# Kernel tuning notes

Measured on AMD Instinct MI355X. Metric: run time of the kernel, lower is better.

Reference implementation:

```python
import jax, jax.numpy as jnp
import numpy as np

N_NODES = 10000
N_EDGES = 160000
F_IN, D1, D2, D_OUT, K = 512, 512, 512, 256, 3


def _gcn_layer(x, row, col, w, W, b, n):
    # PyG GCNConv (improved=False): add self-loops with weight 1, sym norm.
    loop = jnp.arange(n)
    r = jnp.concatenate([row, loop])
    c = jnp.concatenate([col, loop])
    ww = jnp.concatenate([w, jnp.ones((n,), w.dtype)])
    deg = jax.ops.segment_sum(ww, c, num_segments=n)
    dinv = jnp.where(deg > 0, jax.lax.rsqrt(deg), 0.0)
    norm = dinv[r] * ww * dinv[c]              # [E+N]
    h = x @ W                                  # dense GEMM first (as PyG lin)
    out = jax.ops.segment_sum(norm[:, None] * h[r], c, num_segments=n)
    return out + b


def _cheb_layer(x, row, col, w, Wk, b, n):
    # PyG ChebConv, normalization='sym', lambda_max=2.0:
    # L_hat = 2L/lmax - I = -D^{-1/2} A D^{-1/2} (self-loops removed first).
    w0 = jnp.where(row == col, jnp.zeros((), w.dtype), w)  # remove self loops
    deg = jax.ops.segment_sum(w0, row, num_segments=n)
    dinv = jnp.where(deg > 0, jax.lax.rsqrt(deg), 0.0)
    norm = dinv[row] * w0 * dinv[col]          # [E]

    def lhat(z):  # L_hat @ z
        return -jax.ops.segment_sum(norm[:, None] * z[row], col, num_segments=n)

    Tx0 = x
    out = Tx0 @ Wk[0]
    Tx1 = lhat(x)
    out = out + Tx1 @ Wk[1]
    for k in range(2, Wk.shape[0]):            # static K, fine to unroll
        Tx2 = 2.0 * lhat(Tx1) - Tx0
        out = out + Tx2 @ Wk[k]
        Tx0, Tx1 = Tx1, Tx2
    return out + b


def setup_inputs() -> dict:
    key = jax.random.key(0)
    ks = jax.random.split(key, 9)
    x = jax.random.normal(ks[0], (N_NODES, F_IN), dtype=jnp.float32)
    edge_index = jax.random.randint(ks[1], (2, N_EDGES), 0, N_NODES, dtype=jnp.int64)
    edge_weight = jax.random.uniform(ks[2], (N_EDGES,), dtype=jnp.float32)
    s = lambda fan: 1.0 / np.sqrt(fan)
    W1 = jax.random.normal(ks[3], (F_IN, D1), dtype=jnp.float32) * s(F_IN)
    b1 = jnp.zeros((D1,), jnp.float32)
    W2 = jax.random.normal(ks[4], (D1, D2), dtype=jnp.float32) * s(D1)
    b2 = jnp.zeros((D2,), jnp.float32)
    Wc = jax.random.normal(ks[5], (K, D2, D_OUT), dtype=jnp.float32) * s(D2)
    bc = jnp.zeros((D_OUT,), jnp.float32)
    return {"x": x, "edge_index": edge_index, "edge_weight": edge_weight,
            "W1": W1, "b1": b1, "W2": W2, "b2": b2, "Wc": Wc, "bc": bc}


def reference(x, edge_index, edge_weight, W1, b1, W2, b2, Wc, bc):
    row, col = edge_index[0], edge_index[1]
    n = x.shape[0]
    h = jax.nn.celu(_gcn_layer(x, row, col, edge_weight, W1, b1, n))
    h = jax.nn.celu(_gcn_layer(h, row, col, edge_weight, W2, b2, n))
    h = jax.nn.celu(_cheb_layer(h, row, col, edge_weight, Wc, bc, n))
    return h
```

## Files before the change

kernel.cpp:

```cpp
#include <hip/hip_runtime.h>
#include <math.h>

#define N_NODES 10000
#define N_EDGES 160000
#define FDIM    512
#define DOUT    256

typedef unsigned short ushort_t;
typedef unsigned int   uint_t;
typedef __attribute__((ext_vector_type(8))) short bf16x8;
typedef __attribute__((ext_vector_type(4))) float f32x4;

__device__ inline ushort_t f2bf(float f) {
    uint_t u = __float_as_uint(f);
    u += 0x7fffu + ((u >> 16) & 1u);
    return (ushort_t)(u >> 16);
}
__device__ inline void bf2f8(uint4 u, float* v) {
    v[0] = __uint_as_float(u.x << 16); v[1] = __uint_as_float(u.x & 0xffff0000u);
    v[2] = __uint_as_float(u.y << 16); v[3] = __uint_as_float(u.y & 0xffff0000u);
    v[4] = __uint_as_float(u.z << 16); v[5] = __uint_as_float(u.z & 0xffff0000u);
    v[6] = __uint_as_float(u.w << 16); v[7] = __uint_as_float(u.w & 0xffff0000u);
}
__device__ inline uint4 f2bf8v(const float* v) {
    uint4 u;
    u.x = (uint_t)f2bf(v[0]) | ((uint_t)f2bf(v[1]) << 16);
    u.y = (uint_t)f2bf(v[2]) | ((uint_t)f2bf(v[3]) << 16);
    u.z = (uint_t)f2bf(v[4]) | ((uint_t)f2bf(v[5]) << 16);
    u.w = (uint_t)f2bf(v[6]) | ((uint_t)f2bf(v[7]) << 16);
    return u;
}
__device__ inline void gld_lds16(const ushort_t* g, ushort_t* l) {
    __builtin_amdgcn_global_load_lds(
        (const __attribute__((address_space(1))) unsigned int*)g,
        (__attribute__((address_space(3))) unsigned int*)l,
        16, 0, 0);
}

__global__ void k_edge_deg(const int* __restrict__ row, const int* __restrict__ col,
                           const float* __restrict__ w,
                           float* deg_g, float* deg_c, int* counts, int E) {
    int e = blockIdx.x * blockDim.x + threadIdx.x;
    if (e >= E) return;
    int r = row[e], c = col[e];
    float wv = w[e];
    atomicAdd(&deg_g[c], wv);
    if (r != c) atomicAdd(&deg_c[r], wv);
    atomicAdd(&counts[c], 1);
}

__global__ __launch_bounds__(256) void k_dinv_scan1(
    const float* __restrict__ deg_g, const float* __restrict__ deg_c,
    float* __restrict__ dinv_g, float* __restrict__ dinv_c,
    const int* __restrict__ counts, int* __restrict__ rp,
    int* __restrict__ part, int n)
{
    __shared__ int s[256];
    int tid = threadIdx.x;
    int i = blockIdx.x * 256 + tid;
    if (i < n) {
        dinv_g[i] = rsqrtf(deg_g[i] + 1.0f);
        float d = deg_c[i];
        dinv_c[i] = d > 0.f ? rsqrtf(d) : 0.f;
    }
    int v = (i < n) ? counts[i] : 0;
    s[tid] = v;
    __syncthreads();
    for (int o = 1; o < 256; o <<= 1) {
        int t = (tid >= o) ? s[tid - o] : 0;
        __syncthreads();
        s[tid] += t;
        __syncthreads();
    }
    if (i < n) rp[i] = s[tid] - v;
    if (tid == 255) part[blockIdx.x] = s[255];
}

__global__ __launch_bounds__(64) void k_scan2(int* __restrict__ part,
                                              int* __restrict__ rp, int nb, int n) {
    int tid = threadIdx.x;
    int v = (tid < nb) ? part[tid] : 0;
    int x = v;
    for (int o = 1; o < 64; o <<= 1) {
        int y = __shfl_up(x, o, 64);
        if (tid >= o) x += y;
    }
    if (tid < nb) part[tid] = x - v;
    if (tid == 63) rp[n] = x;
}

__global__ __launch_bounds__(256) void k_scan3(int* __restrict__ rp,
                                               const int* __restrict__ part, int n) {
    int i = blockIdx.x * 256 + threadIdx.x;
    if (i < n) rp[i] += part[blockIdx.x];
}

__global__ void k_fill(const int* __restrict__ row, const int* __restrict__ col,
                       const float* __restrict__ w,
                       const float* __restrict__ dinv_g, const float* __restrict__ dinv_c,
                       const int* __restrict__ rp, int* __restrict__ fill,
                       int2* __restrict__ eg, int2* __restrict__ ec, int E) {
    int e = blockIdx.x * blockDim.x + threadIdx.x;
    if (e >= E) return;
    int r = row[e], c = col[e];
    float wv = w[e];
    float ng = dinv_g[r] * wv * dinv_g[c];
    float w0 = (r == c) ? 0.f : wv;
    float nc = -(dinv_c[r] * w0 * dinv_c[c]);
    int pos = rp[c] + atomicAdd(&fill[c], 1);
    eg[pos] = make_int2(r, __float_as_int(ng));
    ec[pos] = make_int2(r, __float_as_int(nc));
}

#define CNX (N_NODES * FDIM / 4)
#define CNW (FDIM * FDIM)
#define CNC (3 * FDIM * DOUT)

__global__ void k_conv(const float* __restrict__ x,  ushort_t* __restrict__ xb,
                       const float* __restrict__ W1, ushort_t* __restrict__ W1t,
                       const float* __restrict__ W2, ushort_t* __restrict__ W2t,
                       const float* __restrict__ Wc, ushort_t* __restrict__ Wct) {
    int t = blockIdx.x * blockDim.x + threadIdx.x;
    if (t < CNX) {
        float4 v = *(const float4*)(x + (size_t)t * 4);
        uint2 p;
        p.x = (uint_t)f2bf(v.x) | ((uint_t)f2bf(v.y) << 16);
        p.y = (uint_t)f2bf(v.z) | ((uint_t)f2bf(v.w) << 16);
        *(uint2*)(xb + (size_t)t * 4) = p;
    } else if (t < CNX + 2 * CNW) {
        int iw = t - CNX;
        const float* W = W1; ushort_t* Wt = W1t;
        if (iw >= CNW) { iw -= CNW; W = W2; Wt = W2t; }
        int n = iw & (FDIM - 1), k = iw >> 9;
        Wt[(size_t)n * FDIM + k] = f2bf(W[(size_t)k * FDIM + n]);
    } else if (t < CNX + 2 * CNW + CNC) {
        int ic = t - CNX - 2 * CNW;
        int n = ic & 255, d = (ic >> 8) & 511, kk = ic >> 17;
        Wct[(size_t)n * 1536 + kk * 512 + d] = f2bf(Wc[((size_t)kk * 512 + d) * 256 + n]);
    }
}

template<int TBM>
__global__ __launch_bounds__(256) void k_mgemm(
    const ushort_t* __restrict__ A, int lda,
    const ushort_t* __restrict__ Bt, int ldb,
    int M, int K, int N, int nbx, int nbS,
    const float* __restrict__ bias,
    ushort_t* __restrict__ outB, float* __restrict__ outF)
{
    constexpr int MI = TBM / 32;
    constexpr int AI = TBM / 64;
    __shared__ ushort_t As[TBM * 32];
    __shared__ ushort_t Bs[128 * 32];

    int id = blockIdx.x;
    int by = (id >> 3) & ((1 << nbS) - 1);
    int bx = ((id >> (3 + nbS)) << 3) | (id & 7);
    if (bx >= nbx) return;

    const int tid  = threadIdx.x;
    const int w    = tid >> 6;
    const int lane = tid & 63;
    const int l15  = lane & 15;
    const int quad = lane >> 4;
    const int bm = bx * TBM, bn = by * 128;
    const int wm = (w & 1) * (TBM / 2);
    const int wn = (w >> 1) * 64;

    const int sr = lane >> 2;
    const int sc = (lane & 3) * 8;
    const ushort_t* ag[AI]; ushort_t* al[AI];
#pragma unroll
    for (int i = 0; i < AI; ++i) {
        int rt = (w * AI + i) * 16 + sr;
        int ar = min(bm + rt, M - 1);
        ag[i] = A + (size_t)ar * lda + sc;
        al[i] = As + rt * 32 + sc;
    }
    const ushort_t* bg[2]; ushort_t* bl[2];
#pragma unroll
    for (int i = 0; i < 2; ++i) {
        int rt = (w * 2 + i) * 16 + sr;
        bg[i] = Bt + (size_t)(bn + rt) * ldb + sc;
        bl[i] = Bs + rt * 32 + sc;
    }

    f32x4 acc[MI][4] = {};

    for (int k0 = 0; k0 < K; k0 += 32) {
        __syncthreads();
#pragma unroll
        for (int i = 0; i < AI; ++i) gld_lds16(ag[i] + k0, al[i]);
#pragma unroll
        for (int i = 0; i < 2; ++i)  gld_lds16(bg[i] + k0, bl[i]);
        __syncthreads();
        bf16x8 af[MI], bfr[4];
#pragma unroll
        for (int i = 0; i < MI; ++i)
            af[i] = *(const bf16x8*)(As + (wm + i * 16 + l15) * 32 + quad * 8);
#pragma unroll
        for (int j = 0; j < 4; ++j)
            bfr[j] = *(const bf16x8*)(Bs + (wn + j * 16 + l15) * 32 + quad * 8);
#pragma unroll
        for (int i = 0; i < MI; ++i)
#pragma unroll
            for (int j = 0; j < 4; ++j)
                acc[i][j] = __builtin_amdgcn_mfma_f32_16x16x32_bf16(af[i], bfr[j], acc[i][j], 0, 0, 0);
    }

#pragma unroll
    for (int i = 0; i < MI; ++i) {
        int rowb = bm + wm + i * 16 + quad * 4;
#pragma unroll
        for (int j = 0; j < 4; ++j) {
            int col = bn + wn + j * 16 + l15;
#pragma unroll
            for (int r = 0; r < 4; ++r) {
                int rr = rowb + r;
                if (rr < M) {
                    float v = acc[i][j][r];
                    if (outF) {
                        v += bias[col];
                        v = v > 0.f ? v : expm1f(v);
                        outF[(size_t)rr * N + col] = v;
                    } else {
                        outB[(size_t)rr * N + col] = f2bf(v);
                    }
                }
            }
        }
    }
}

__global__ __launch_bounds__(256) void k_sagg(
    const ushort_t* __restrict__ h, int hs,
    const int2* __restrict__ er, const int* __restrict__ rp,
    const float* __restrict__ dinv_g, const float* __restrict__ bias,
    const ushort_t* __restrict__ other, int os,
    ushort_t* __restrict__ out, int outs,
    float sA, float sB, int gcn)
{
    const int id  = blockIdx.x;
    const int sl  = id & 7;
    const int tid = threadIdx.x;
    const int c   = (id >> 3) * 32 + (tid >> 3);
    if (c >= N_NODES) return;
    const int fb = sl * 64 + ((tid & 7) << 3);

    float acc[8] = {0.f, 0.f, 0.f, 0.f, 0.f, 0.f, 0.f, 0.f};
    int e = rp[c];
    const int e1 = rp[c + 1];
    for (; e + 2 <= e1; e += 2) {
        int2 p0 = er[e], p1 = er[e + 1];
        uint4 u0 = *(const uint4*)(h + (size_t)p0.x * hs + fb);
        uint4 u1 = *(const uint4*)(h + (size_t)p1.x * hs + fb);
        float n0 = __int_as_float(p0.y), n1 = __int_as_float(p1.y);
        float v0[8], v1[8];
        bf2f8(u0, v0); bf2f8(u1, v1);
#pragma unroll
        for (int i = 0; i < 8; ++i) {
            acc[i] = fmaf(n0, v0[i], acc[i]);
            acc[i] = fmaf(n1, v1[i], acc[i]);
        }
    }
    if (e < e1) {
        int2 p = er[e];
        uint4 u = *(const uint4*)(h + (size_t)p.x * hs + fb);
        float nv = __int_as_float(p.y);
        float v[8]; bf2f8(u, v);
#pragma unroll
        for (int i = 0; i < 8; ++i) acc[i] = fmaf(nv, v[i], acc[i]);
    }

    float r[8];
    if (gcn) {
        float dv = dinv_g[c];
        float d2 = dv * dv;
        uint4 u = *(const uint4*)(h + (size_t)c * hs + fb);
        float v[8]; bf2f8(u, v);
#pragma unroll
        for (int i = 0; i < 8; ++i) {
            float xv = fmaf(d2, v[i], acc[i]) + bias[fb + i];
            r[i] = xv > 0.f ? xv : expm1f(xv);
        }
    } else {
        float o[8] = {0.f, 0.f, 0.f, 0.f, 0.f, 0.f, 0.f, 0.f};
        if (other) {
            uint4 u = *(const uint4*)(other + (size_t)c * os + fb);
            bf2f8(u, o);
        }
#pragma unroll
        for (int i = 0; i < 8; ++i) r[i] = fmaf(sA, acc[i], sB * o[i]);
    }
    *(uint4*)(out + (size_t)c * outs + fb) = f2bf8v(r);
}


extern "C" void kernel_launch(void* const* d_in, const int* in_sizes, int n_in,
                              void* d_out, int out_size, void* d_ws, size_t ws_size,
                              hipStream_t stream) {
    const float* x  = (const float*)d_in[0];
    const int*   ei = (const int*)d_in[1];
    const float* ew = (const float*)d_in[2];
    const float* W1 = (const float*)d_in[3];
    const float* b1 = (const float*)d_in[4];
    const float* W2 = (const float*)d_in[5];
    const float* b2 = (const float*)d_in[6];
    const float* Wc = (const float*)d_in[7];
    const float* bc = (const float*)d_in[8];
    float* out = (float*)d_out;

    const int* row = ei;
    const int* col = ei + N_EDGES;

    char* ws = (char*)d_ws;
    size_t off = 0;
    auto alloc = [&](size_t bytes) -> void* {
        void* p = ws + off;
        off += (bytes + 255) & ~(size_t)255;
        return p;
    };
    ushort_t* xb   = (ushort_t*)alloc((size_t)N_NODES * FDIM * 2);
    ushort_t* bufA = (ushort_t*)alloc((size_t)N_NODES * FDIM * 2);
    ushort_t* bufB = (ushort_t*)alloc((size_t)N_NODES * FDIM * 2);
    ushort_t* Tbuf = (ushort_t*)alloc((size_t)N_NODES * 3 * FDIM * 2);
    ushort_t* W1t  = (ushort_t*)alloc((size_t)FDIM * FDIM * 2);
    ushort_t* W2t  = (ushort_t*)alloc((size_t)FDIM * FDIM * 2);
    ushort_t* Wct  = (ushort_t*)alloc((size_t)DOUT * 3 * FDIM * 2);
    size_t zs = off;
    float* deg_g  = (float*)alloc((size_t)N_NODES * 4);
    float* deg_c  = (float*)alloc((size_t)N_NODES * 4);
    int*   counts = (int*)alloc((size_t)N_NODES * 4);
    int*   fill   = (int*)alloc((size_t)N_NODES * 4);
    size_t ze = off;
    float* dinv_g = (float*)alloc((size_t)N_NODES * 4);
    float* dinv_c = (float*)alloc((size_t)N_NODES * 4);
    int*   rp     = (int*)alloc((size_t)(N_NODES + 1) * 4);
    int*   part   = (int*)alloc(64 * 4);
    int2*  eg     = (int2*)alloc((size_t)N_EDGES * 8);
    int2*  ec     = (int2*)alloc((size_t)N_EDGES * 8);

    const int TB = 256;
    dim3 edgeGrid((N_EDGES + TB - 1) / TB);
    int nScanB = (N_NODES + 255) / 256;

    hipMemsetAsync(ws + zs, 0, ze - zs, stream);
    k_edge_deg<<<edgeGrid, TB, 0, stream>>>(row, col, ew, deg_g, deg_c, counts, N_EDGES);
    k_dinv_scan1<<<nScanB, 256, 0, stream>>>(deg_g, deg_c, dinv_g, dinv_c, counts, rp, part, N_NODES);
    k_scan2<<<1, 64, 0, stream>>>(part, rp, nScanB, N_NODES);
    k_scan3<<<nScanB, 256, 0, stream>>>(rp, part, N_NODES);
    k_fill<<<edgeGrid, TB, 0, stream>>>(row, col, ew, dinv_g, dinv_c, rp, fill, eg, ec, N_EDGES);

    {
        int tot = CNX + 2 * CNW + CNC;
        k_conv<<<(tot + TB - 1) / TB, TB, 0, stream>>>(x, xb, W1, W1t, W2, W2t, Wc, Wct);
    }

    auto mgemm128 = [&](const ushort_t* A, int lda, const ushort_t* Bt, int ldb,
                        int M, int K, int N, ushort_t* oB) {
        int nbx = (M + 127) / 128, nby = N / 128;
        int nbS = (nby == 4) ? 2 : 1;
        int G = ((nbx + 7) / 8) * 8 * nby;
        k_mgemm<128><<<G, 256, 0, stream>>>(A, lda, Bt, ldb, M, K, N, nbx, nbS,
                                            (const float*)nullptr, oB, (float*)nullptr);
    };

    int saggG = ((N_NODES + 31) / 32) * 8;

    mgemm128(xb, FDIM, W1t, FDIM, N_NODES, FDIM, FDIM, bufA);
    k_sagg<<<saggG, 256, 0, stream>>>(bufA, FDIM, eg, rp, dinv_g, b1,
                                      (const ushort_t*)nullptr, 0,
                                      bufB, FDIM, 1.f, 0.f, 1);
    mgemm128(bufB, FDIM, W2t, FDIM, N_NODES, FDIM, FDIM, bufA);
    k_sagg<<<saggG, 256, 0, stream>>>(bufA, FDIM, eg, rp, dinv_g, b2,
                                      (const ushort_t*)nullptr, 0,
                                      Tbuf, 3 * FDIM, 1.f, 0.f, 1);
    k_sagg<<<saggG, 256, 0, stream>>>(Tbuf, 3 * FDIM, ec, rp,
                                      (const float*)nullptr, (const float*)nullptr,
                                      (const ushort_t*)nullptr, 0,
                                      Tbuf + FDIM, 3 * FDIM, 1.f, 0.f, 0);
    k_sagg<<<saggG, 256, 0, stream>>>(Tbuf + FDIM, 3 * FDIM, ec, rp,
                                      (const float*)nullptr, (const float*)nullptr,
                                      Tbuf, 3 * FDIM,
                                      Tbuf + 2 * FDIM, 3 * FDIM, 2.f, -1.f, 0);

    {
        int nbx = (N_NODES + 63) / 64;
        int G = ((nbx + 7) / 8) * 8 * 2;
        k_mgemm<64><<<G, 256, 0, stream>>>(Tbuf, 3 * FDIM, Wct, 3 * FDIM,
                                           N_NODES, 3 * FDIM, DOUT, nbx, 1,
                                           bc, (ushort_t*)nullptr, out);
    }
}
```

Baseline: 298.0 us.

## Reorder Chebyshev layer to project before propagating and fuse scan kernels

The Chebyshev layer is rewritten algebraically. The input is projected once through concatenated weights [W0-W2, W1, W2] (768 columns), and then two sparse propagations run on 256-wide features in a Horner-style form. The previous version ran two 512-wide propagations and a K=1536 GEMM. The weight conversion now uses tiled LDS transposes, and the two scan kernels are merged into one, which removes a launch. The risk is a different bf16 rounding order, since W0-W2 is computed in fp32 before conversion and the intermediates are bf16.

Measured after the change: 256.1 us. 1.16x faster.

```diff
diff --git a/kernel.cpp b/kernel.cpp
--- a/kernel.cpp
+++ b/kernel.cpp
@@ -5,6 +5,7 @@
 #define N_EDGES 160000
 #define FDIM    512
 #define DOUT    256
+#define NCAT    768
 
 typedef unsigned short ushort_t;
 typedef unsigned int   uint_t;
@@ -76,23 +77,26 @@
     if (tid == 255) part[blockIdx.x] = s[255];
 }
 
-__global__ __launch_bounds__(64) void k_scan2(int* __restrict__ part,
-                                              int* __restrict__ rp, int nb, int n) {
+__global__ __launch_bounds__(256) void k_scan23(int* __restrict__ rp,
+                                                const int* __restrict__ part,
+                                                int nb, int n) {
+    __shared__ int soff[64];
+    __shared__ int stot;
     int tid = threadIdx.x;
-    int v = (tid < nb) ? part[tid] : 0;
-    int x = v;
-    for (int o = 1; o < 64; o <<= 1) {
-        int y = __shfl_up(x, o, 64);
-        if (tid >= o) x += y;
-    }
-    if (tid < nb) part[tid] = x - v;
-    if (tid == 63) rp[n] = x;
-}
-
-__global__ __launch_bounds__(256) void k_scan3(int* __restrict__ rp,
-                                               const int* __restrict__ part, int n) {
-    int i = blockIdx.x * 256 + threadIdx.x;
-    if (i < n) rp[i] += part[blockIdx.x];
+    if (tid < 64) {
+        int v = (tid < nb) ? part[tid] : 0;
+        int x = v;
+        for (int o = 1; o < 64; o <<= 1) {
+            int y = __shfl_up(x, o, 64);
+            if (tid >= o) x += y;
+        }
+        soff[tid] = x - v;
+        if (tid == 63) stot = x;
+    }
+    __syncthreads();
+    int i = blockIdx.x * 256 + tid;
+    if (i < n) rp[i] += soff[blockIdx.x];
+    if (blockIdx.x == 0 && tid == 0) rp[n] = stot;
 }
 
 __global__ void k_fill(const int* __restrict__ row, const int* __restrict__ col,
@@ -112,50 +116,96 @@
     ec[pos] = make_int2(r, __float_as_int(nc));
 }
 
-#define CNX (N_NODES * FDIM / 4)
-#define CNW (FDIM * FDIM)
-#define CNC (3 * FDIM * DOUT)
-
-__global__ void k_conv(const float* __restrict__ x,  ushort_t* __restrict__ xb,
-                       const float* __restrict__ W1, ushort_t* __restrict__ W1t,
-                       const float* __restrict__ W2, ushort_t* __restrict__ W2t,
-                       const float* __restrict__ Wc, ushort_t* __restrict__ Wct) {
-    int t = blockIdx.x * blockDim.x + threadIdx.x;
-    if (t < CNX) {
+#define XB_BLOCKS 5000
+
+__global__ __launch_bounds__(256) void k_conv(
+    const float* __restrict__ x,  ushort_t* __restrict__ xb,
+    const float* __restrict__ W1, ushort_t* __restrict__ W1t,
+    const float* __restrict__ W2, ushort_t* __restrict__ W2t,
+    const float* __restrict__ Wc, ushort_t* __restrict__ Wcatt)
+{
+    int b = blockIdx.x;
+    int tid = threadIdx.x;
+    if (b < XB_BLOCKS) {
+        int t = b * 256 + tid;
         float4 v = *(const float4*)(x + (size_t)t * 4);
         uint2 p;
         p.x = (uint_t)f2bf(v.x) | ((uint_t)f2bf(v.y) << 16);
         p.y = (uint_t)f2bf(v.z) | ((uint_t)f2bf(v.w) << 16);
         *(uint2*)(xb + (size_t)t * 4) = p;
-    } else if (t < CNX + 2 * CNW) {
-        int iw = t - CNX;
-        const float* W = W1; ushort_t* Wt = W1t;
-        if (iw >= CNW) { iw -= CNW; W = W2; Wt = W2t; }
-        int n = iw & (FDIM - 1), k = iw >> 9;
-        Wt[(size_t)n * FDIM + k] = f2bf(W[(size_t)k * FDIM + n]);
-    } else if (t < CNX + 2 * CNW + CNC) {
-        int ic = t - CNX - 2 * CNW;
-        int n = ic & 255, d = (ic >> 8) & 511, kk = ic >> 17;
-        Wct[(size_t)n * 1536 + kk * 512 + d] = f2bf(Wc[((size_t)kk * 512 + d) * 256 + n]);
-    }
-}
-
-template<int TBM>
+        return;
+    }
+    b -= XB_BLOCKS;
+    __shared__ float tile[64][65];
+    const float* src; const float* src2 = nullptr;
+    ushort_t* dst; int kt, ntG, srcld;
+    if (b < 64) {
+        kt = b >> 3; ntG = b & 7; srcld = FDIM;
+        src = W1 + (size_t)(kt * 64) * FDIM + ntG * 64;
+        dst = W1t;
+    } else if (b < 128) {
+        int bb = b - 64;
+        kt = bb >> 3; ntG = bb & 7; srcld = FDIM;
+        src = W2 + (size_t)(kt * 64) * FDIM + ntG * 64;
+        dst = W2t;
+    } else {
+        int bb = b - 128;
+        ntG = bb / 8; kt = bb % 8; srcld = DOUT;
+        int s = ntG >> 2;
+        int nl = (ntG & 3) * 64;
+        if (s == 0) {
+            src  = Wc + (size_t)(kt * 64) * DOUT + nl;
+            src2 = Wc + (size_t)2 * FDIM * DOUT + (size_t)(kt * 64) * DOUT + nl;
+        } else if (s == 1) {
+            src  = Wc + (size_t)1 * FDIM * DOUT + (size_t)(kt * 64) * DOUT + nl;
+        } else {
+            src  = Wc + (size_t)2 * FDIM * DOUT + (size_t)(kt * 64) * DOUT + nl;
+        }
+        dst = Wcatt;
+    }
+    {
+        int r = tid >> 2, c0 = (tid & 3) * 16;
+        const float* sp = src + (size_t)r * srcld + c0;
+#pragma unroll
+        for (int q = 0; q < 4; ++q) {
+            float4 a = *(const float4*)(sp + q * 4);
+            if (src2) {
+                float4 bsub = *(const float4*)(src2 + (size_t)r * srcld + c0 + q * 4);
+                a.x -= bsub.x; a.y -= bsub.y; a.z -= bsub.z; a.w -= bsub.w;
+            }
+            tile[r][c0 + q * 4 + 0] = a.x;
+            tile[r][c0 + q * 4 + 1] = a.y;
+            tile[r][c0 + q * 4 + 2] = a.z;
+            tile[r][c0 + q * 4 + 3] = a.w;
+        }
+    }
+    __syncthreads();
+    {
+        int n = tid >> 2, k0 = (tid & 3) * 16;
+        float v[16];
+#pragma unroll
+        for (int i = 0; i < 16; ++i) v[i] = tile[k0 + i][n];
+        uint4 u0 = f2bf8v(v);
+        uint4 u1 = f2bf8v(v + 8);
+        ushort_t* dp = dst + (size_t)(ntG * 64 + n) * FDIM + kt * 64 + k0;
+        *(uint4*)dp = u0;
+        *(uint4*)(dp + 8) = u1;
+    }
+}
+
 __global__ __launch_bounds__(256) void k_mgemm(
     const ushort_t* __restrict__ A, int lda,
     const ushort_t* __restrict__ Bt, int ldb,
-    int M, int K, int N, int nbx, int nbS,
-    const float* __restrict__ bias,
-    ushort_t* __restrict__ outB, float* __restrict__ outF)
+    int M, int K, int N, int nbx, int nby,
+    ushort_t* __restrict__ outB)
 {
-    constexpr int MI = TBM / 32;
-    constexpr int AI = TBM / 64;
-    __shared__ ushort_t As[TBM * 32];
+    __shared__ ushort_t As[128 * 32];
     __shared__ ushort_t Bs[128 * 32];
 
     int id = blockIdx.x;
-    int by = (id >> 3) & ((1 << nbS) - 1);
-    int bx = ((id >> (3 + nbS)) << 3) | (id & 7);
+    int j = id & 7, t = id >> 3;
+    int by = t % nby;
+    int bx = (t / nby) * 8 + j;
     if (bx >= nbx) return;
 
     const int tid  = threadIdx.x;
@@ -163,16 +213,16 @@
     const int lane = tid & 63;
     const int l15  = lane & 15;
     const int quad = lane >> 4;
-    const int bm = bx * TBM, bn = by * 128;
-    const int wm = (w & 1) * (TBM / 2);
+    const int bm = bx * 128, bn = by * 128;
+    const int wm = (w & 1) * 64;
     const int wn = (w >> 1) * 64;
 
     const int sr = lane >> 2;
     const int sc = (lane & 3) * 8;
-    const ushort_t* ag[AI]; ushort_t* al[AI];
-#pragma unroll
-    for (int i = 0; i < AI; ++i) {
-        int rt = (w * AI + i) * 16 + sr;
+    const ushort_t* ag[2]; ushort_t* al[2];
+#pragma unroll
+    for (int i = 0; i < 2; ++i) {
+        int rt = (w * 2 + i) * 16 + sr;
         int ar = min(bm + rt, M - 1);
         ag[i] = A + (size_t)ar * lda + sc;
         al[i] = As + rt * 32 + sc;
@@ -185,75 +235,69 @@
         bl[i] = Bs + rt * 32 + sc;
     }
 
-    f32x4 acc[MI][4] = {};
+    f32x4 acc[4][4] = {};
 
     for (int k0 = 0; k0 < K; k0 += 32) {
         __syncthreads();
 #pragma unroll
-        for (int i = 0; i < AI; ++i) gld_lds16(ag[i] + k0, al[i]);
-#pragma unroll
-        for (int i = 0; i < 2; ++i)  gld_lds16(bg[i] + k0, bl[i]);
+        for (int i = 0; i < 2; ++i) gld_lds16(ag[i] + k0, al[i]);
+#pragma unroll
+        for (int i = 0; i < 2; ++i) gld_lds16(bg[i] + k0, bl[i]);
         __syncthreads();
-        bf16x8 af[MI], bfr[4];
-#pragma unroll
-        for (int i = 0; i < MI; ++i)
+        bf16x8 af[4], bfr[4];
+#pragma unroll
+        for (int i = 0; i < 4; ++i)
             af[i] = *(const bf16x8*)(As + (wm + i * 16 + l15) * 32 + quad * 8);
 #pragma unroll
-        for (int j = 0; j < 4; ++j)
-            bfr[j] = *(const bf16x8*)(Bs + (wn + j * 16 + l15) * 32 + quad * 8);
-#pragma unroll
-        for (int i = 0; i < MI; ++i)
-#pragma unroll
-            for (int j = 0; j < 4; ++j)
-                acc[i][j] = __builtin_amdgcn_mfma_f32_16x16x32_bf16(af[i], bfr[j], acc[i][j], 0, 0, 0);
-    }
-
-#pragma unroll
-    for (int i = 0; i < MI; ++i) {
+        for (int jj = 0; jj < 4; ++jj)
+            bfr[jj] = *(const bf16x8*)(Bs + (wn + jj * 16 + l15) * 32 + quad * 8);
+#pragma unroll
+        for (int i = 0; i < 4; ++i)
+#pragma unroll
+            for (int jj = 0; jj < 4; ++jj)
+                acc[i][jj] = __builtin_amdgcn_mfma_f32_16x16x32_bf16(af[i], bfr[jj], acc[i][jj], 0, 0, 0);
+    }
+
+#pragma unroll
+    for (int i = 0; i < 4; ++i) {
         int rowb = bm + wm + i * 16 + quad * 4;
 #pragma unroll
-        for (int j = 0; j < 4; ++j) {
-            int col = bn + wn + j * 16 + l15;
+        for (int jj = 0; jj < 4; ++jj) {
+            int col = bn + wn + jj * 16 + l15;
 #pragma unroll
             for (int r = 0; r < 4; ++r) {
                 int rr = rowb + r;
-                if (rr < M) {
-                    float v = acc[i][j][r];
-                    if (outF) {
-                        v += bias[col];
-                        v = v > 0.f ? v : expm1f(v);
-                        outF[(size_t)rr * N + col] = v;
-                    } else {
-                        outB[(size_t)rr * N + col] = f2bf(v);
-                    }
-                }
+                if (rr < M)
+                    outB[(size_t)rr * N + col] = f2bf(acc[i][jj][r]);
             }
         }
     }
 }
 
+template<int SL>
 __global__ __launch_bounds__(256) void k_sagg(
-    const ushort_t* __restrict__ h, int hs,
+    const ushort_t* __restrict__ h, int hs, int hoff,
     const int2* __restrict__ er, const int* __restrict__ rp,
-    const float* __restrict__ dinv_g, const float* __restrict__ bias,
-    const ushort_t* __restrict__ other, int os,
-    ushort_t* __restrict__ out, int outs,
-    float sA, float sB, int gcn)
+    const float* __restrict__ dinv_g,
+    const ushort_t* __restrict__ other, int os, int ooff, float sB,
+    const float* __restrict__ bias, float sA,
+    ushort_t* __restrict__ outB, float* __restrict__ outF, int outs, int celu)
 {
     const int id  = blockIdx.x;
-    const int sl  = id & 7;
+    const int sl  = id % SL;
     const int tid = threadIdx.x;
-    const int c   = (id >> 3) * 32 + (tid >> 3);
+    const int c   = (id / SL) * 32 + (tid >> 3);
     if (c >= N_NODES) return;
-    const int fb = sl * 64 + ((tid & 7) << 3);
+    const int f = sl * 64 + ((tid & 7) << 3);
+    const ushort_t* hp = h + hoff + f;
 
     float acc[8] = {0.f, 0.f, 0.f, 0.f, 0.f, 0.f, 0.f, 0.f};
     int e = rp[c];
     const int e1 = rp[c + 1];
     for (; e + 2 <= e1; e += 2) {
         int2 p0 = er[e], p1 = er[e + 1];
-        uint4 u0 = *(const uint4*)(h + (size_t)p0.x * hs + fb);
-        uint4 u1 = *(const uint4*)(h + (size_t)p1.x * hs + fb);
+        uint4 u0 = *(const uint4*)(hp + (size_t)p0.x * hs);
+        uint4 u1 = *(const uint4*)(hp + (size_t)p1.x * hs);
         float n0 = __int_as_float(p0.y), n1 = __int_as_float(p1.y);
         float v0[8], v1[8];
         bf2f8(u0, v0); bf2f8(u1, v1);
@@ -265,34 +309,45 @@
     }
     if (e < e1) {
         int2 p = er[e];
-        uint4 u = *(const uint4*)(h + (size_t)p.x * hs + fb);
+        uint4 u = *(const uint4*)(hp + (size_t)p.x * hs);
         float nv = __int_as_float(p.y);
         float v[8]; bf2f8(u, v);
 #pragma unroll
         for (int i = 0; i < 8; ++i) acc[i] = fmaf(nv, v[i], acc[i]);
     }
 
-    float r[8];
-    if (gcn) {
+    if (dinv_g) {
         float dv = dinv_g[c];
         float d2 = dv * dv;
-        uint4 u = *(const uint4*)(h + (size_t)c * hs + fb);
+        uint4 u = *(const uint4*)(hp + (size_t)c * hs);
         float v[8]; bf2f8(u, v);
 #pragma unroll
-        for (int i = 0; i < 8; ++i) {
-            float xv = fmaf(d2, v[i], acc[i]) + bias[fb + i];
-            r[i] = xv > 0.f ? xv : expm1f(xv);
-        }
+        for (int i = 0; i < 8; ++i) acc[i] = fmaf(d2, v[i], acc[i]);
+    }
+    float r[8];
+#pragma unroll
+    for (int i = 0; i < 8; ++i) r[i] = sA * acc[i];
+    if (other) {
+        uint4 u = *(const uint4*)(other + (size_t)c * os + ooff + f);
+        float o[8]; bf2f8(u, o);
+#pragma unroll
+        for (int i = 0; i < 8; ++i) r[i] = fmaf(sB, o[i], r[i]);
+    }
+    if (bias) {
+#pragma unroll
+        for (int i = 0; i < 8; ++i) r[i] += bias[f + i];
+    }
+    if (celu) {
+#pragma unroll
+        for (int i = 0; i < 8; ++i) r[i] = r[i] > 0.f ? r[i] : expm1f(r[i]);
+    }
+    if (outF) {
+        float* op = outF + (size_t)c * outs + f;
+        *(float4*)op       = make_float4(r[0], r[1], r[2], r[3]);
+        *(float4*)(op + 4) = make_float4(r[4], r[5], r[6], r[7]);
     } else {
-        float o[8] = {0.f, 0.f, 0.f, 0.f, 0.f, 0.f, 0.f, 0.f};
-        if (other) {
-            uint4 u = *(const uint4*)(other + (size_t)c * os + fb);
-            bf2f8(u, o);
-        }
-#pragma unroll
-        for (int i = 0; i < 8; ++i) r[i] = fmaf(sA, acc[i], sB * o[i]);
-    }
-    *(uint4*)(out + (size_t)c * outs + fb) = f2bf8v(r);
+        *(uint4*)(outB + (size_t)c * outs + f) = f2bf8v(r);
+    }
 }
 
 
@@ -320,18 +375,19 @@
         off += (bytes + 255) & ~(size_t)255;
         return p;
     };
-    ushort_t* xb   = (ushort_t*)alloc((size_t)N_NODES * FDIM * 2);
-    ushort_t* bufA = (ushort_t*)alloc((size_t)N_NODES * FDIM * 2);
-    ushort_t* bufB = (ushort_t*)alloc((size_t)N_NODES * FDIM * 2);
-    ushort_t* Tbuf = (ushort_t*)alloc((size_t)N_NODES * 3 * FDIM * 2);
-    ushort_t* W1t  = (ushort_t*)alloc((size_t)FDIM * FDIM * 2);
-    ushort_t* W2t  = (ushort_t*)alloc((size_t)FDIM * FDIM * 2);
-    ushort_t* Wct  = (ushort_t*)alloc((size_t)DOUT * 3 * FDIM * 2);
+    ushort_t* xb    = (ushort_t*)alloc((size_t)N_NODES * FDIM * 2);
+    ushort_t* bufA  = (ushort_t*)alloc((size_t)N_NODES * FDIM * 2);
+    ushort_t* bufB  = (ushort_t*)alloc((size_t)N_NODES * FDIM * 2);
+    ushort_t* Y     = (ushort_t*)alloc((size_t)N_NODES * NCAT * 2);
+    ushort_t* P     = (ushort_t*)alloc((size_t)N_NODES * DOUT * 2);
+    ushort_t* W1t   = (ushort_t*)alloc((size_t)FDIM * FDIM * 2);
+    ushort_t* W2t   = (ushort_t*)alloc((size_t)FDIM * FDIM * 2);
+    ushort_t* Wcatt = (ushort_t*)alloc((size_t)NCAT * FDIM * 2);
     size_t zs = off;
     float* deg_g  = (float*)alloc((size_t)N_NODES * 4);
     float* deg_c  = (float*)alloc((size_t)N_NODES * 4);
     int*   counts = (int*)alloc((size_t)N_NODES * 4);
-    int*   fill   = (int*)alloc((size_t)N_NODES * 4);
+    int*   fillb  = (int*)alloc((size_t)N_NODES * 4);
     size_t ze = off;
     float* dinv_g = (float*)alloc((size_t)N_NODES * 4);
     float* dinv_c = (float*)alloc((size_t)N_NODES * 4);
@@ -347,48 +403,36 @@
     hipMemsetAsync(ws + zs, 0, ze - zs, stream);
     k_edge_deg<<<edgeGrid, TB, 0, stream>>>(row, col, ew, deg_g, deg_c, counts, N_EDGES);
     k_dinv_scan1<<<nScanB, 256, 0, stream>>>(deg_g, deg_c, dinv_g, dinv_c, counts, rp, part, N_NODES);
-    k_scan2<<<1, 64, 0, stream>>>(part, rp, nScanB, N_NODES);
-    k_scan3<<<nScanB, 256, 0, stream>>>(rp, part, N_NODES);
-    k_fill<<<edgeGrid, TB, 0, stream>>>(row, col, ew, dinv_g, dinv_c, rp, fill, eg, ec, N_EDGES);
-
-    {
-        int tot = CNX + 2 * CNW + CNC;
-        k_conv<<<(tot + TB - 1) / TB, TB, 0, stream>>>(x, xb, W1, W1t, W2, W2t, Wc, Wct);
-    }
-
-    auto mgemm128 = [&](const ushort_t* A, int lda, const ushort_t* Bt, int ldb,
-                        int M, int K, int N, ushort_t* oB) {
-        int nbx = (M + 127) / 128, nby = N / 128;
-        int nbS = (nby == 4) ? 2 : 1;
-        int G = ((nbx + 7) / 8) * 8 * nby;
-        k_mgemm<128><<<G, 256, 0, stream>>>(A, lda, Bt, ldb, M, K, N, nbx, nbS,
-                                            (const float*)nullptr, oB, (float*)nullptr);
+    k_scan23<<<nScanB, 256, 0, stream>>>(rp, part, nScanB, N_NODES);
+    k_fill<<<edgeGrid, TB, 0, stream>>>(row, col, ew, dinv_g, dinv_c, rp, fillb, eg, ec, N_EDGES);
+
+    k_conv<<<XB_BLOCKS + 224, 256, 0, stream>>>(x, xb, W1, W1t, W2, W2t, Wc, Wcatt);
+
+    auto mgemm = [&](const ushort_t* A, const ushort_t* Bt, int N, ushort_t* oB) {
+        int nbx = (N_NODES + 127) / 128, nby = N / 128;
+        int G = 8 * (((nbx + 7) / 8) * nby);
+        k_mgemm<<<G, 256, 0, stream>>>(A, FDIM, Bt, FDIM, N_NODES, FDIM, N, nbx, nby, oB);
     };
-
-    int saggG = ((N_NODES + 31) / 32) * 8;
-
-    mgemm128(xb, FDIM, W1t, FDIM, N_NODES, FDIM, FDIM, bufA);
-    k_sagg<<<saggG, 256, 0, stream>>>(bufA, FDIM, eg, rp, dinv_g, b1,
-                                      (const ushort_t*)nullptr, 0,
-                                      bufB, FDIM, 1.f, 0.f, 1);
-    mgemm128(bufB, FDIM, W2t, FDIM, N_NODES, FDIM, FDIM, bufA);
-    k_sagg<<<saggG, 256, 0, stream>>>(bufA, FDIM, eg, rp, dinv_g, b2,
-                                      (const ushort_t*)nullptr, 0,
-                                      Tbuf, 3 * FDIM, 1.f, 0.f, 1);
-    k_sagg<<<saggG, 256, 0, stream>>>(Tbuf, 3 * FDIM, ec, rp,
-                                      (const float*)nullptr, (const float*)nullptr,
-                                      (const ushort_t*)nullptr, 0,
-                                      Tbuf + FDIM, 3 * FDIM, 1.f, 0.f, 0);
-    k_sagg<<<saggG, 256, 0, stream>>>(Tbuf + FDIM, 3 * FDIM, ec, rp,
-                                      (const float*)nullptr, (const float*)nullptr,
-                                      Tbuf, 3 * FDIM,
-                                      Tbuf + 2 * FDIM, 3 * FDIM, 2.f, -1.f, 0);
-
-    {
-        int nbx = (N_NODES + 63) / 64;
-        int G = ((nbx + 7) / 8) * 8 * 2;
-        k_mgemm<64><<<G, 256, 0, stream>>>(Tbuf, 3 * FDIM, Wct, 3 * FDIM,
-                                           N_NODES, 3 * FDIM, DOUT, nbx, 1,
-                                           bc, (ushort_t*)nullptr, out);
-    }
-}
+    int g8 = ((N_NODES + 31) / 32) * 8;
+    int g4 = ((N_NODES + 31) / 32) * 4;
+
+    mgemm(xb, W1t, FDIM, bufA);
+    k_sagg<8><<<g8, 256, 0, stream>>>(bufA, FDIM, 0, eg, rp, dinv_g,
+                                      (const ushort_t*)nullptr, 0, 0, 0.f,
+                                      b1, 1.f, bufB, (float*)nullptr, FDIM, 1);
+    mgemm(bufB, W2t, FDIM, bufA);
+    k_sagg<8><<<g8, 256, 0, stream>>>(bufA, FDIM, 0, eg, rp, dinv_g,
+                                      (const ushort_t*)nullptr, 0, 0, 0.f,
+                                      b2, 1.f, bufB, (float*)nullptr, FDIM, 1);
+    mgemm(bufB, Wcatt, NCAT, Y);
+    k_sagg<4><<<g4, 256, 0, stream>>>(Y, NCAT, 2 * DOUT, ec, rp,
+                                      (const float*)nullptr,
+                                      Y, NCAT, DOUT, 1.f,
+                                      (const float*)nullptr, 2.f,
+                                      P, (float*)nullptr, DOUT, 0);
+    k_sagg<4><<<g4, 256, 0, stream>>>(P, DOUT, 0, ec, rp,
+                                      (const float*)nullptr,
+                                      Y, NCAT, 0, 1.f,
+                                      bc, 1.f,
+                                      (ushort_t*)nullptr, out, DOUT, 1);
+}
```
